# Performance work log

Measured on AMD Instinct MI355X. Metric: run time of the kernel, lower is better.

## Reference

```python
import jax, jax.numpy as jnp
import numpy as np

B, T, D, H = 2, 2048, 2048, 16
HD = D // H  # 128


def setup_inputs() -> dict:
    key = jax.random.key(0)
    ks = jax.random.split(key, 9)
    s = 0.02
    return {
        "x": jax.random.normal(ks[0], (B, T, D), jnp.float32),
        "Wq": jax.random.normal(ks[1], (D, D), jnp.float32) * s,
        "bq": jnp.zeros((D,), jnp.float32),
        "Wk": jax.random.normal(ks[2], (D, HD), jnp.float32) * s,
        "bk": jnp.zeros((HD,), jnp.float32),
        "Wv": jax.random.normal(ks[3], (D, HD), jnp.float32) * s,
        "bv": jnp.zeros((HD,), jnp.float32),
        "Wo": jax.random.normal(ks[4], (D, D), jnp.float32) * s,
        "bo": jnp.zeros((D,), jnp.float32),
    }


def reference(x, Wq, bq, Wk, bk, Wv, bv, Wo, bo):
    Bx, Tx, Dx = x.shape
    hd = Wk.shape[1]
    h = Dx // hd
    # Q: (B, T, D) -> (B, H, T, hd)
    q = (x @ Wq + bq).reshape(Bx, Tx, h, hd).transpose(0, 2, 1, 3)
    # K, V: single shared head (B, T, hd) -> (B, 1, T, hd) via broadcast in einsum
    k = x @ Wk + bk  # (B, T, hd)
    v = x @ Wv + bv  # (B, T, hd)
    scale = 1.0 / jnp.sqrt(jnp.asarray(hd, x.dtype))
    # scores: (B, H, Tq, Tk); shared K broadcasts across all H query heads
    scores = jnp.einsum("bhqd,bkd->bhqk", q, k) * scale
    causal = jnp.tril(jnp.ones((Tx, Tx), bool))  # (Tq, Tk)
    scores = jnp.where(causal, scores, jnp.asarray(-1e9, scores.dtype))
    attn = jax.nn.softmax(scores, axis=-1)
    # out: (B, H, Tq, hd) with shared V
    out = jnp.einsum("bhqk,bkd->bhqd", attn, v)
    out = out.transpose(0, 2, 1, 3).reshape(Bx, Tx, Dx)
    return out @ Wo + bo
```

## Files before the change

### kernel.cpp

```cpp
#include <hip/hip_runtime.h>
#include <cstdint>
#include <cstddef>

#define Bq 2
#define Tq 2048
#define Dq 2048
#define Hq 16
#define HDq 128

using f32x4  = __attribute__((ext_vector_type(4))) float;
using short8 = __attribute__((ext_vector_type(8))) short;
typedef unsigned short ushort_t;

#define QSC 0.12751741772f

#define GLOAD_LDS16(gp, lp)                                                        \
  __builtin_amdgcn_global_load_lds((const __attribute__((address_space(1))) void*)(gp), \
                                   (__attribute__((address_space(3))) void*)(lp), 16, 0, 0)

__device__ inline ushort_t f2bf(float f) {
  uint32_t u = __float_as_uint(f);
  uint32_t r = (u + 0x7FFFu + ((u >> 16) & 1u)) >> 16;
  return (ushort_t)r;
}

__device__ inline uint32_t cvt_pk_bf16(float a, float b) {
  uint32_t r;
  asm("v_cvt_pk_bf16_f32 %0, %1, %2" : "=v"(r) : "v"(a), "v"(b));
  return r;
}

__global__ void cast_f32_bf16(const float* __restrict__ in, ushort_t* __restrict__ out, int n4) {
  int stride = gridDim.x * blockDim.x;
  for (int i = blockIdx.x * blockDim.x + threadIdx.x; i < n4; i += stride) {
    float4 v = reinterpret_cast<const float4*>(in)[i];
    ushort4 u;
    u.x = f2bf(v.x); u.y = f2bf(v.y); u.z = f2bf(v.z); u.w = f2bf(v.w);
    reinterpret_cast<ushort4*>(out)[i] = u;
  }
}

__global__ __launch_bounds__(512) void cast_transpose(
    const float* __restrict__ in, ushort_t* __restrict__ out,
    int R, int C, int row_off) {
  __shared__ float tile[64][65];
  int c0 = blockIdx.x * 64, r0 = blockIdx.y * 64;
  int tx = threadIdx.x, ty = threadIdx.y;
#pragma unroll
  for (int i = ty; i < 64; i += 8)
    tile[i][tx] = in[(size_t)(r0 + i) * C + c0 + tx];
  __syncthreads();
#pragma unroll
  for (int i = ty; i < 64; i += 8)
    out[(size_t)(row_off + c0 + i) * R + r0 + tx] = f2bf(tile[tx][i]);
}

template <int OUT_MODE>
__global__ __launch_bounds__(256, 3) void gemm_bt(
    const ushort_t* __restrict__ A, const ushort_t* __restrict__ BT,
    const float* __restrict__ bias, void* __restrict__ Cout,
    int M, int N, int K, int NXT,
    ushort_t* __restrict__ Kout, ushort_t* __restrict__ VTout,
    const float* __restrict__ bias2, const float* __restrict__ bias3) {
  constexpr int BM = 128, BN = 128, BK = 64;
  __shared__ ushort_t As[BM * BK];
  __shared__ ushort_t Bs[BN * BK];
  const int tid = threadIdx.x;
  const int wave = tid >> 6, lane = tid & 63;
  const int wr = wave >> 1, wc = wave & 1;
  const int nwg = gridDim.x;
  const int orig = (blockIdx.x & 7) * (nwg >> 3) + (blockIdx.x >> 3);
  const int m0 = (orig / NXT) * BM, n0 = (orig % NXT) * BN;
  const int lrow = lane & 15;
  const int kswz0 = (((lane >> 4) ^ (lrow & 7)) << 3);
  const int kswz1 = (((4 + (lane >> 4)) ^ (lrow & 7)) << 3);

  int srcoff[4], dstoff[4];
#pragma unroll
  for (int p = 0; p < 4; ++p) {
    const int byteoff = p * 4096 + wave * 1024;
    const int e = (byteoff >> 1) + lane * 8;
    const int r = e >> 6, c = e & 63;
    const int cs = (((c >> 3) ^ (r & 7)) << 3);
    srcoff[p] = r * K + cs;
    dstoff[p] = byteoff;
  }

  f32x4 acc[4][4] = {};

  for (int k0 = 0; k0 < K; k0 += BK) {
#pragma unroll
    for (int p = 0; p < 4; ++p) {
      GLOAD_LDS16(A + (size_t)m0 * K + k0 + srcoff[p], (char*)As + dstoff[p]);
      GLOAD_LDS16(BT + (size_t)n0 * K + k0 + srcoff[p], (char*)Bs + dstoff[p]);
    }
    __syncthreads();
#pragma unroll
    for (int kk = 0; kk < 2; ++kk) {
      const int ksw = kk ? kswz1 : kswz0;
      short8 af[4], bfr[4];
#pragma unroll
      for (int i = 0; i < 4; ++i)
        af[i] = *(const short8*)&As[(wr * 64 + i * 16 + lrow) * BK + ksw];
#pragma unroll
      for (int i = 0; i < 4; ++i)
        bfr[i] = *(const short8*)&Bs[(wc * 64 + i * 16 + lrow) * BK + ksw];
#pragma unroll
      for (int mi = 0; mi < 4; ++mi)
#pragma unroll
        for (int ni = 0; ni < 4; ++ni)
          acc[mi][ni] = __builtin_amdgcn_mfma_f32_16x16x32_bf16(af[mi], bfr[ni], acc[mi][ni], 0, 0, 0);
    }
    __syncthreads();
  }

#pragma unroll
  for (int mi = 0; mi < 4; ++mi) {
#pragma unroll
    for (int ni = 0; ni < 4; ++ni) {
      int rbase = m0 + wr * 64 + mi * 16 + (lane >> 4) * 4;
      int col = n0 + wc * 64 + ni * 16 + lrow;
#pragma unroll
      for (int jj = 0; jj < 4; ++jj) {
        int r = rbase + jj;
        float v = acc[mi][ni][jj];
        if (OUT_MODE == 1) {
          ((float*)Cout)[(size_t)r * N + col] = v + bias[col];
        } else {
          if (col < Dq) {
            ((ushort_t*)Cout)[(size_t)r * Dq + col] = f2bf((v + bias[col]) * QSC);
          } else if (col < Dq + HDq) {
            int d = col - Dq;
            Kout[(size_t)r * HDq + d] = f2bf(v + bias2[d]);
          } else {
            int d = col - Dq - HDq;
            int b = r >> 11, t = r & (Tq - 1);
            VTout[((size_t)b * HDq + d) * Tq + t] = f2bf(v + bias3[d]);
          }
        }
      }
    }
  }
}

__global__ __launch_bounds__(256, 2) void mqa_attn(
    const ushort_t* __restrict__ Qb, const ushort_t* __restrict__ Kb,
    const ushort_t* __restrict__ VTb, ushort_t* __restrict__ Ab) {
  const int bid = blockIdx.x;
  const int bh = bid & 31;
  const int b = bh >> 4, h = bh & 15;
  const int qt = (bid < 256) ? (15 - (bid >> 5)) : ((bid - 256) >> 5);
  const int NT = 2 * qt + 2;

  const int wave = threadIdx.x >> 6, lane = threadIdx.x & 63;
  const int lrow = lane & 15, lk8 = (lane >> 4) * 8;
  const int rb = (lane >> 4) * 4;

  __shared__ ushort_t Ks[2][64 * 128];
  __shared__ ushort_t Vs[2][128 * 64];
  __shared__ ushort_t Pl[4][32 * 64];

  const size_t vtb = (size_t)b * HDq * Tq;
  const size_t kbb = (size_t)b * Tq * HDq;

  size_t kgoff[4], vgoff[4];
#pragma unroll
  for (int rnd = 0; rnd < 4; ++rnd) {
    const int base = rnd * 4096 + wave * 1024;
    const int L = base + lane * 16;
    const int r = L >> 8, c = L & 255;
    kgoff[rnd] = (size_t)r * HDq + ((c ^ ((r & 7) << 4)) >> 1);
    const int r2 = L >> 7, c2 = L & 127;
    vgoff[rnd] = (size_t)r2 * Tq + ((c2 ^ ((r2 & 7) << 4)) >> 1);
  }

  auto stage = [&](int kt, int buf) {
#pragma unroll
    for (int rnd = 0; rnd < 4; ++rnd) {
      const int base = rnd * 4096 + wave * 1024;
      GLOAD_LDS16(Kb + kbb + (size_t)kt * 64 * HDq + kgoff[rnd],
                  (char*)Ks + buf * 16384 + base);
      GLOAD_LDS16(VTb + vtb + kt * 64 + vgoff[rnd],
                  (char*)Vs + buf * 16384 + base);
    }
  };

  short8 qf[2][4];
#pragma unroll
  for (int mi = 0; mi < 2; ++mi) {
    const size_t qrow = (size_t)(b * Tq + qt * 128 + wave * 32 + mi * 16 + lrow) * Dq + h * HDq;
#pragma unroll
    for (int dc = 0; dc < 4; ++dc)
      qf[mi][dc] = *(const short8*)(Qb + qrow + dc * 32 + lk8);
  }

  f32x4 o[2][8] = {};
  float l_run[2][4] = {};

  stage(0, 0);
  __syncthreads();

  int cur = 0;
  for (int s = 0; s < NT; ++s) {
    if (s + 1 < NT) stage(s + 1, cur ^ 1);
    const int kt = s;

    f32x4 sc[2][4] = {};
#pragma unroll
    for (int ni = 0; ni < 4; ++ni) {
      const int R = ni * 16 + lrow;
      short8 kf[4];
#pragma unroll
      for (int dc = 0; dc < 4; ++dc) {
        const int C = (dc * 64 + lk8 * 2) ^ ((R & 7) << 4);
        kf[dc] = *(const short8*)((const char*)Ks + cur * 16384 + R * 256 + C);
      }
#pragma unroll
      for (int dc = 0; dc < 4; ++dc) {
        sc[0][ni] = __builtin_amdgcn_mfma_f32_16x16x32_bf16(qf[0][dc], kf[dc], sc[0][ni], 0, 0, 0);
        sc[1][ni] = __builtin_amdgcn_mfma_f32_16x16x32_bf16(qf[1][dc], kf[dc], sc[1][ni], 0, 0, 0);
      }
    }

#pragma unroll
    for (int mi = 0; mi < 2; ++mi) {
      const int qr0 = qt * 128 + wave * 32 + mi * 16;
      if (kt * 64 + 63 > qr0) {
        const int qg = qr0 + rb;
#pragma unroll
        for (int ni = 0; ni < 4; ++ni) {
          const int kg = kt * 64 + ni * 16 + lrow;
#pragma unroll
          for (int jj = 0; jj < 4; ++jj)
            if (kg > qg + jj) sc[mi][ni][jj] = -1e30f;
        }
      }
    }

#pragma unroll
    for (int mi = 0; mi < 2; ++mi) {
#pragma unroll
      for (int ni = 0; ni < 4; ++ni) {
        float p0 = exp2f(fminf(sc[mi][ni][0], 24.f) - 8.f);
        float p1 = exp2f(fminf(sc[mi][ni][1], 24.f) - 8.f);
        float p2 = exp2f(fminf(sc[mi][ni][2], 24.f) - 8.f);
        float p3 = exp2f(fminf(sc[mi][ni][3], 24.f) - 8.f);
        l_run[mi][0] += p0; l_run[mi][1] += p1;
        l_run[mi][2] += p2; l_run[mi][3] += p3;
        const uint32_t u01 = cvt_pk_bf16(p0, p1);
        const uint32_t u23 = cvt_pk_bf16(p2, p3);
        const int col = ni * 16 + lrow;
        const int rowb = mi * 16 + rb;
        Pl[wave][(rowb + 0) * 64 + (col ^ ((rb << 2) ^ 0))]  = (ushort_t)u01;
        Pl[wave][(rowb + 1) * 64 + (col ^ ((rb << 2) ^ 8))]  = (ushort_t)(u01 >> 16);
        Pl[wave][(rowb + 2) * 64 + (col ^ ((rb << 2) ^ 16))] = (ushort_t)u23;
        Pl[wave][(rowb + 3) * 64 + (col ^ ((rb << 2) ^ 24))] = (ushort_t)(u23 >> 16);
      }
    }

    short8 pa[2][2];
    const int fsw = ((lrow & 12) << 2) ^ ((lrow & 3) << 3);
#pragma unroll
    for (int mi = 0; mi < 2; ++mi)
#pragma unroll
      for (int kc = 0; kc < 2; ++kc)
        pa[mi][kc] = *(const short8*)&Pl[wave][(mi * 16 + lrow) * 64 + ((kc * 32 + lk8) ^ fsw)];
#pragma unroll
    for (int df = 0; df < 8; ++df) {
      const int R = df * 16 + lrow;
#pragma unroll
      for (int kc = 0; kc < 2; ++kc) {
        const int C = (kc * 64 + lk8 * 2) ^ ((R & 7) << 4);
        short8 vf = *(const short8*)((const char*)Vs + cur * 16384 + R * 128 + C);
        o[0][df] = __builtin_amdgcn_mfma_f32_16x16x32_bf16(pa[0][kc], vf, o[0][df], 0, 0, 0);
        o[1][df] = __builtin_amdgcn_mfma_f32_16x16x32_bf16(pa[1][kc], vf, o[1][df], 0, 0, 0);
      }
    }

    __syncthreads();
    cur ^= 1;
  }

#pragma unroll
  for (int mi = 0; mi < 2; ++mi) {
    float inv[4];
#pragma unroll
    for (int jj = 0; jj < 4; ++jj) {
      float l = l_run[mi][jj];
#pragma unroll
      for (int off = 1; off < 16; off <<= 1) l += __shfl_xor(l, off, 64);
      inv[jj] = 1.f / l;
    }
    const size_t orow = (size_t)(b * Tq + qt * 128 + wave * 32 + mi * 16 + rb);
#pragma unroll
    for (int df = 0; df < 8; ++df) {
      const int col = h * HDq + df * 16 + lrow;
#pragma unroll
      for (int jj = 0; jj < 4; ++jj)
        Ab[(orow + jj) * Dq + col] = f2bf(o[mi][df][jj] * inv[jj]);
    }
  }
}

extern "C" void kernel_launch(void* const* d_in, const int* in_sizes, int n_in,
                              void* d_out, int out_size, void* d_ws, size_t ws_size,
                              hipStream_t stream) {
  const float* x  = (const float*)d_in[0];
  const float* Wq = (const float*)d_in[1];
  const float* bq = (const float*)d_in[2];
  const float* Wk = (const float*)d_in[3];
  const float* bk = (const float*)d_in[4];
  const float* Wv = (const float*)d_in[5];
  const float* bv = (const float*)d_in[6];
  const float* Wo = (const float*)d_in[7];
  const float* bo = (const float*)d_in[8];
  float* out = (float*)d_out;

  char* ws = (char*)d_ws;
  ushort_t* xb     = (ushort_t*)(ws);
  ushort_t* WqkvT  = (ushort_t*)(ws + 16777216);
  ushort_t* WoT    = (ushort_t*)(ws + 26214400);
  ushort_t* Qb     = (ushort_t*)(ws + 34603008);
  ushort_t* Kb     = (ushort_t*)(ws + 51380224);
  ushort_t* VTb    = (ushort_t*)(ws + 52428800);
  ushort_t* Ab     = (ushort_t*)(ws + 53477376);

  const int MT = Bq * Tq;

  cast_f32_bf16<<<2048, 256, 0, stream>>>(x, xb, MT * Dq / 4);
  cast_transpose<<<dim3(Dq / 64, Dq / 64), dim3(64, 8), 0, stream>>>(Wq, WqkvT, Dq, Dq, 0);
  cast_transpose<<<dim3(HDq / 64, Dq / 64), dim3(64, 8), 0, stream>>>(Wk, WqkvT, Dq, HDq, 2048);
  cast_transpose<<<dim3(HDq / 64, Dq / 64), dim3(64, 8), 0, stream>>>(Wv, WqkvT, Dq, HDq, 2176);
  cast_transpose<<<dim3(Dq / 64, Dq / 64), dim3(64, 8), 0, stream>>>(Wo, WoT, Dq, Dq, 0);

  gemm_bt<3><<<(2304 / 128) * (MT / 128), 256, 0, stream>>>(
      xb, WqkvT, bq, Qb, MT, 2304, Dq, 2304 / 128, Kb, VTb, bk, bv);

  mqa_attn<<<512, 256, 0, stream>>>(Qb, Kb, VTb, Ab);

  gemm_bt<1><<<(Dq / 128) * (MT / 128), 256, 0, stream>>>(
      Ab, WoT, bo, out, MT, Dq, Dq, Dq / 128, nullptr, nullptr, nullptr, nullptr);
}
```

Measured before the change: 200.4 us.

## Shrink attention tiles to 64 query rows, single-buffer K/V, fuse weight prep

Each attention block now handles 64 query rows (one 16-row MFMA tile per wave) instead of 128, doubling the grid to 1024 blocks and raising launch bounds to 4 waves per SIMD. K/V staging drops from double to single buffering, with K for the next tile loaded after the QK step and V after the PV step, split across barriers. Causal masking now runs only on the last tile. The four weight cast-transpose launches are merged into one 3D-grid kernel. The aim is more occupancy and less per-block imbalance, at the cost of more K/V reloads per query row and less overlap from single buffering.

After: 191.3 us, median of 3. 4.5% less time.

```diff
diff --git a/kernel.cpp b/kernel.cpp
--- a/kernel.cpp
+++ b/kernel.cpp
@@ -40,19 +40,30 @@
   }
 }
 
-__global__ __launch_bounds__(512) void cast_transpose(
-    const float* __restrict__ in, ushort_t* __restrict__ out,
-    int R, int C, int row_off) {
+__global__ __launch_bounds__(512) void prep_weights(
+    const float* __restrict__ Wq, const float* __restrict__ Wk,
+    const float* __restrict__ Wv, const float* __restrict__ Wo,
+    ushort_t* __restrict__ WqkvT, ushort_t* __restrict__ WoT) {
+  const int z = blockIdx.z;
+  const float* in;
+  ushort_t* out;
+  int C, row_off;
+  if (z == 0)      { in = Wq; out = WqkvT; C = Dq;  row_off = 0; }
+  else if (z == 1) { in = Wo; out = WoT;   C = Dq;  row_off = 0; }
+  else if (z == 2) { in = Wk; out = WqkvT; C = HDq; row_off = 2048; }
+  else             { in = Wv; out = WqkvT; C = HDq; row_off = 2176; }
+  const int c0 = blockIdx.x * 64;
+  if (c0 >= C) return;
   __shared__ float tile[64][65];
-  int c0 = blockIdx.x * 64, r0 = blockIdx.y * 64;
-  int tx = threadIdx.x, ty = threadIdx.y;
+  const int r0 = blockIdx.y * 64;
+  const int tx = threadIdx.x, ty = threadIdx.y;
 #pragma unroll
   for (int i = ty; i < 64; i += 8)
     tile[i][tx] = in[(size_t)(r0 + i) * C + c0 + tx];
   __syncthreads();
 #pragma unroll
   for (int i = ty; i < 64; i += 8)
-    out[(size_t)(row_off + c0 + i) * R + r0 + tx] = f2bf(tile[tx][i]);
+    out[(size_t)(row_off + c0 + i) * Dq + r0 + tx] = f2bf(tile[tx][i]);
 }
 
 template <int OUT_MODE>
@@ -143,69 +154,69 @@
   }
 }
 
-__global__ __launch_bounds__(256, 2) void mqa_attn(
+__global__ __launch_bounds__(256, 4) void mqa_attn(
     const ushort_t* __restrict__ Qb, const ushort_t* __restrict__ Kb,
     const ushort_t* __restrict__ VTb, ushort_t* __restrict__ Ab) {
   const int bid = blockIdx.x;
+  const int jt = 31 - (bid >> 5);
   const int bh = bid & 31;
   const int b = bh >> 4, h = bh & 15;
-  const int qt = (bid < 256) ? (15 - (bid >> 5)) : ((bid - 256) >> 5);
-  const int NT = 2 * qt + 2;
+  const int qrow0 = jt * 64;
+  const int NT = jt + 1;
 
   const int wave = threadIdx.x >> 6, lane = threadIdx.x & 63;
   const int lrow = lane & 15, lk8 = (lane >> 4) * 8;
   const int rb = (lane >> 4) * 4;
 
-  __shared__ ushort_t Ks[2][64 * 128];
-  __shared__ ushort_t Vs[2][128 * 64];
-  __shared__ ushort_t Pl[4][32 * 64];
+  __shared__ ushort_t Ks[64 * 128];
+  __shared__ ushort_t Vs[128 * 64];
+  __shared__ ushort_t Pl[4][16 * 64];
 
   const size_t vtb = (size_t)b * HDq * Tq;
   const size_t kbb = (size_t)b * Tq * HDq;
 
-  size_t kgoff[4], vgoff[4];
+  int kgoff[4], vgoff[4], lbase[4];
 #pragma unroll
   for (int rnd = 0; rnd < 4; ++rnd) {
     const int base = rnd * 4096 + wave * 1024;
     const int L = base + lane * 16;
     const int r = L >> 8, c = L & 255;
-    kgoff[rnd] = (size_t)r * HDq + ((c ^ ((r & 7) << 4)) >> 1);
+    kgoff[rnd] = r * HDq + ((c ^ ((r & 7) << 4)) >> 1);
     const int r2 = L >> 7, c2 = L & 127;
-    vgoff[rnd] = (size_t)r2 * Tq + ((c2 ^ ((r2 & 7) << 4)) >> 1);
-  }
-
-  auto stage = [&](int kt, int buf) {
-#pragma unroll
-    for (int rnd = 0; rnd < 4; ++rnd) {
-      const int base = rnd * 4096 + wave * 1024;
-      GLOAD_LDS16(Kb + kbb + (size_t)kt * 64 * HDq + kgoff[rnd],
-                  (char*)Ks + buf * 16384 + base);
-      GLOAD_LDS16(VTb + vtb + kt * 64 + vgoff[rnd],
-                  (char*)Vs + buf * 16384 + base);
-    }
+    vgoff[rnd] = r2 * Tq + ((c2 ^ ((r2 & 7) << 4)) >> 1);
+    lbase[rnd] = base;
+  }
+
+  auto stageK = [&](int kt) {
+    const ushort_t* kp = Kb + kbb + (size_t)kt * 64 * HDq;
+#pragma unroll
+    for (int rnd = 0; rnd < 4; ++rnd)
+      GLOAD_LDS16(kp + kgoff[rnd], (char*)Ks + lbase[rnd]);
   };
-
-  short8 qf[2][4];
-#pragma unroll
-  for (int mi = 0; mi < 2; ++mi) {
-    const size_t qrow = (size_t)(b * Tq + qt * 128 + wave * 32 + mi * 16 + lrow) * Dq + h * HDq;
+  auto stageV = [&](int kt) {
+    const ushort_t* vp = VTb + vtb + kt * 64;
+#pragma unroll
+    for (int rnd = 0; rnd < 4; ++rnd)
+      GLOAD_LDS16(vp + vgoff[rnd], (char*)Vs + lbase[rnd]);
+  };
+
+  short8 qf[4];
+  {
+    const size_t qrow = (size_t)(b * Tq + qrow0 + wave * 16 + lrow) * Dq + h * HDq;
 #pragma unroll
     for (int dc = 0; dc < 4; ++dc)
-      qf[mi][dc] = *(const short8*)(Qb + qrow + dc * 32 + lk8);
-  }
-
-  f32x4 o[2][8] = {};
-  float l_run[2][4] = {};
-
-  stage(0, 0);
+      qf[dc] = *(const short8*)(Qb + qrow + dc * 32 + lk8);
+  }
+
+  f32x4 o[8] = {};
+  float l_run[4] = {};
+
+  stageK(0);
+  stageV(0);
   __syncthreads();
 
-  int cur = 0;
   for (int s = 0; s < NT; ++s) {
-    if (s + 1 < NT) stage(s + 1, cur ^ 1);
-    const int kt = s;
-
-    f32x4 sc[2][4] = {};
+    f32x4 sc[4] = {};
 #pragma unroll
     for (int ni = 0; ni < 4; ++ni) {
       const int R = ni * 16 + lrow;
@@ -213,92 +224,78 @@
 #pragma unroll
       for (int dc = 0; dc < 4; ++dc) {
         const int C = (dc * 64 + lk8 * 2) ^ ((R & 7) << 4);
-        kf[dc] = *(const short8*)((const char*)Ks + cur * 16384 + R * 256 + C);
+        kf[dc] = *(const short8*)((const char*)Ks + R * 256 + C);
       }
 #pragma unroll
-      for (int dc = 0; dc < 4; ++dc) {
-        sc[0][ni] = __builtin_amdgcn_mfma_f32_16x16x32_bf16(qf[0][dc], kf[dc], sc[0][ni], 0, 0, 0);
-        sc[1][ni] = __builtin_amdgcn_mfma_f32_16x16x32_bf16(qf[1][dc], kf[dc], sc[1][ni], 0, 0, 0);
+      for (int dc = 0; dc < 4; ++dc)
+        sc[ni] = __builtin_amdgcn_mfma_f32_16x16x32_bf16(qf[dc], kf[dc], sc[ni], 0, 0, 0);
+    }
+
+    __syncthreads();
+    if (s + 1 < NT) stageK(s + 1);
+
+    if (s == NT - 1) {
+      const int qg = qrow0 + wave * 16 + rb;
+#pragma unroll
+      for (int ni = 0; ni < 4; ++ni) {
+        const int kg = s * 64 + ni * 16 + lrow;
+#pragma unroll
+        for (int jj = 0; jj < 4; ++jj)
+          if (kg > qg + jj) sc[ni][jj] = -1e30f;
       }
     }
 
 #pragma unroll
-    for (int mi = 0; mi < 2; ++mi) {
-      const int qr0 = qt * 128 + wave * 32 + mi * 16;
-      if (kt * 64 + 63 > qr0) {
-        const int qg = qr0 + rb;
-#pragma unroll
-        for (int ni = 0; ni < 4; ++ni) {
-          const int kg = kt * 64 + ni * 16 + lrow;
-#pragma unroll
-          for (int jj = 0; jj < 4; ++jj)
-            if (kg > qg + jj) sc[mi][ni][jj] = -1e30f;
-        }
-      }
-    }
-
-#pragma unroll
-    for (int mi = 0; mi < 2; ++mi) {
-#pragma unroll
-      for (int ni = 0; ni < 4; ++ni) {
-        float p0 = exp2f(fminf(sc[mi][ni][0], 24.f) - 8.f);
-        float p1 = exp2f(fminf(sc[mi][ni][1], 24.f) - 8.f);
-        float p2 = exp2f(fminf(sc[mi][ni][2], 24.f) - 8.f);
-        float p3 = exp2f(fminf(sc[mi][ni][3], 24.f) - 8.f);
-        l_run[mi][0] += p0; l_run[mi][1] += p1;
-        l_run[mi][2] += p2; l_run[mi][3] += p3;
-        const uint32_t u01 = cvt_pk_bf16(p0, p1);
-        const uint32_t u23 = cvt_pk_bf16(p2, p3);
-        const int col = ni * 16 + lrow;
-        const int rowb = mi * 16 + rb;
-        Pl[wave][(rowb + 0) * 64 + (col ^ ((rb << 2) ^ 0))]  = (ushort_t)u01;
-        Pl[wave][(rowb + 1) * 64 + (col ^ ((rb << 2) ^ 8))]  = (ushort_t)(u01 >> 16);
-        Pl[wave][(rowb + 2) * 64 + (col ^ ((rb << 2) ^ 16))] = (ushort_t)u23;
-        Pl[wave][(rowb + 3) * 64 + (col ^ ((rb << 2) ^ 24))] = (ushort_t)(u23 >> 16);
-      }
-    }
-
-    short8 pa[2][2];
+    for (int ni = 0; ni < 4; ++ni) {
+      float p0 = exp2f(fminf(sc[ni][0], 24.f) - 8.f);
+      float p1 = exp2f(fminf(sc[ni][1], 24.f) - 8.f);
+      float p2 = exp2f(fminf(sc[ni][2], 24.f) - 8.f);
+      float p3 = exp2f(fminf(sc[ni][3], 24.f) - 8.f);
+      l_run[0] += p0; l_run[1] += p1; l_run[2] += p2; l_run[3] += p3;
+      const uint32_t u01 = cvt_pk_bf16(p0, p1);
+      const uint32_t u23 = cvt_pk_bf16(p2, p3);
+      const int col = ni * 16 + lrow;
+      Pl[wave][(rb + 0) * 64 + (col ^ ((rb << 2) ^ 0))]  = (ushort_t)u01;
+      Pl[wave][(rb + 1) * 64 + (col ^ ((rb << 2) ^ 8))]  = (ushort_t)(u01 >> 16);
+      Pl[wave][(rb + 2) * 64 + (col ^ ((rb << 2) ^ 16))] = (ushort_t)u23;
+      Pl[wave][(rb + 3) * 64 + (col ^ ((rb << 2) ^ 24))] = (ushort_t)(u23 >> 16);
+    }
+
+    short8 pa[2];
     const int fsw = ((lrow & 12) << 2) ^ ((lrow & 3) << 3);
 #pragma unroll
-    for (int mi = 0; mi < 2; ++mi)
-#pragma unroll
-      for (int kc = 0; kc < 2; ++kc)
-        pa[mi][kc] = *(const short8*)&Pl[wave][(mi * 16 + lrow) * 64 + ((kc * 32 + lk8) ^ fsw)];
+    for (int kc = 0; kc < 2; ++kc)
+      pa[kc] = *(const short8*)&Pl[wave][lrow * 64 + ((kc * 32 + lk8) ^ fsw)];
 #pragma unroll
     for (int df = 0; df < 8; ++df) {
       const int R = df * 16 + lrow;
 #pragma unroll
       for (int kc = 0; kc < 2; ++kc) {
         const int C = (kc * 64 + lk8 * 2) ^ ((R & 7) << 4);
-        short8 vf = *(const short8*)((const char*)Vs + cur * 16384 + R * 128 + C);
-        o[0][df] = __builtin_amdgcn_mfma_f32_16x16x32_bf16(pa[0][kc], vf, o[0][df], 0, 0, 0);
-        o[1][df] = __builtin_amdgcn_mfma_f32_16x16x32_bf16(pa[1][kc], vf, o[1][df], 0, 0, 0);
+        short8 vf = *(const short8*)((const char*)Vs + R * 128 + C);
+        o[df] = __builtin_amdgcn_mfma_f32_16x16x32_bf16(pa[kc], vf, o[df], 0, 0, 0);
       }
     }
 
     __syncthreads();
-    cur ^= 1;
-  }
-
-#pragma unroll
-  for (int mi = 0; mi < 2; ++mi) {
-    float inv[4];
-#pragma unroll
-    for (int jj = 0; jj < 4; ++jj) {
-      float l = l_run[mi][jj];
-#pragma unroll
-      for (int off = 1; off < 16; off <<= 1) l += __shfl_xor(l, off, 64);
-      inv[jj] = 1.f / l;
-    }
-    const size_t orow = (size_t)(b * Tq + qt * 128 + wave * 32 + mi * 16 + rb);
-#pragma unroll
-    for (int df = 0; df < 8; ++df) {
-      const int col = h * HDq + df * 16 + lrow;
-#pragma unroll
-      for (int jj = 0; jj < 4; ++jj)
-        Ab[(orow + jj) * Dq + col] = f2bf(o[mi][df][jj] * inv[jj]);
-    }
+    if (s + 1 < NT) stageV(s + 1);
+  }
+
+  float inv[4];
+#pragma unroll
+  for (int jj = 0; jj < 4; ++jj) {
+    float l = l_run[jj];
+#pragma unroll
+    for (int off = 1; off < 16; off <<= 1) l += __shfl_xor(l, off, 64);
+    inv[jj] = 1.f / l;
+  }
+  const size_t orow = (size_t)(b * Tq + qrow0 + wave * 16 + rb);
+#pragma unroll
+  for (int df = 0; df < 8; ++df) {
+    const int col = h * HDq + df * 16 + lrow;
+#pragma unroll
+    for (int jj = 0; jj < 4; ++jj)
+      Ab[(orow + jj) * Dq + col] = f2bf(o[df][jj] * inv[jj]);
   }
 }
 
@@ -328,15 +325,12 @@
   const int MT = Bq * Tq;
 
   cast_f32_bf16<<<2048, 256, 0, stream>>>(x, xb, MT * Dq / 4);
-  cast_transpose<<<dim3(Dq / 64, Dq / 64), dim3(64, 8), 0, stream>>>(Wq, WqkvT, Dq, Dq, 0);
-  cast_transpose<<<dim3(HDq / 64, Dq / 64), dim3(64, 8), 0, stream>>>(Wk, WqkvT, Dq, HDq, 2048);
-  cast_transpose<<<dim3(HDq / 64, Dq / 64), dim3(64, 8), 0, stream>>>(Wv, WqkvT, Dq, HDq, 2176);
-  cast_transpose<<<dim3(Dq / 64, Dq / 64), dim3(64, 8), 0, stream>>>(Wo, WoT, Dq, Dq, 0);
+  prep_weights<<<dim3(32, 32, 4), dim3(64, 8), 0, stream>>>(Wq, Wk, Wv, Wo, WqkvT, WoT);
 
   gemm_bt<3><<<(2304 / 128) * (MT / 128), 256, 0, stream>>>(
       xb, WqkvT, bq, Qb, MT, 2304, Dq, 2304 / 128, Kb, VTb, bk, bv);
 
-  mqa_attn<<<512, 256, 0, stream>>>(Qb, Kb, VTb, Ab);
+  mqa_attn<<<1024, 256, 0, stream>>>(Qb, Kb, VTb, Ab);
 
   gemm_bt<1><<<(Dq / 128) * (MT / 128), 256, 0, stream>>>(
       Ab, WoT, bo, out, MT, Dq, Dq, Dq / 128, nullptr, nullptr, nullptr, nullptr);
```
